# Optimization experiments

Measured on AMD Instinct MI355X. Metric: run time of the kernel, lower is better.

The kernel has to match this reference:

```python
import jax, jax.numpy as jnp
import numpy as np

N = 50000
E = 800000
IN_FEATS = 256
NUM_HEADS = 4
OUT_FEATS = 64
NUM_ETYPES = 8
ALPHA = 100.0
NEG_SLOPE_ATTN = 0.2   # self.leaky_relu
NEG_SLOPE_EW = 0.01    # nn.LeakyReLU() default, applied to edge weights


def leaky_relu(x, slope):
    return jnp.where(x >= 0, x, slope * x)


def setup_inputs() -> dict:
    key = jax.random.key(0)
    ks = jax.random.split(key, 8)
    feat = jax.random.normal(ks[0], (N, IN_FEATS), dtype=jnp.float32)
    src = jax.random.randint(ks[1], (E,), 0, N, dtype=jnp.int32)
    dst = jax.random.randint(ks[2], (E,), 0, N, dtype=jnp.int32)
    # etypes are 1-indexed in the original code (edge_weight[edge_feats - 1])
    edge_feats = jax.random.randint(ks[3], (E,), 1, NUM_ETYPES + 1, dtype=jnp.int32)
    # parameters (xavier-normal-ish init for weights; edge_weight = 1/alpha)
    fc_w = jax.random.normal(ks[4], (NUM_HEADS * OUT_FEATS, IN_FEATS), dtype=jnp.float32) * 0.05
    attn_l = jax.random.normal(ks[5], (1, NUM_HEADS, OUT_FEATS), dtype=jnp.float32) * 0.1
    attn_r = jax.random.normal(ks[6], (1, NUM_HEADS, OUT_FEATS), dtype=jnp.float32) * 0.1
    edge_weight = jnp.full((NUM_ETYPES, NUM_HEADS), 1.0 / ALPHA, dtype=jnp.float32)
    return {"feat": feat, "src": src, "dst": dst, "edge_feats": edge_feats,
            "fc_w": fc_w, "attn_l": attn_l, "attn_r": attn_r, "edge_weight": edge_weight}


def reference(feat, src, dst, edge_feats, fc_w, attn_l, attn_r, edge_weight):
    # feat: [N, F_in] -> ft: [N, H, D]
    ft = (feat @ fc_w.T).reshape(-1, NUM_HEADS, OUT_FEATS)
    el = jnp.einsum('nhd,ohd->nh', ft, attn_l)  # [N, H]
    er = jnp.einsum('nhd,ohd->nh', ft, attn_r)  # [N, H]
    # edge-type weights (1-indexed), scaled & leaky-relu'd
    ew = leaky_relu(edge_weight * ALPHA, NEG_SLOPE_EW)  # [T, H]
    ee = ew[edge_feats - 1]                              # [E, H]
    # per-edge logits: u_add_v, times edge weight, leaky relu
    e = leaky_relu((el[src] + er[dst]) * ee, NEG_SLOPE_ATTN)  # [E, H]
    # edge softmax grouped by destination node
    emax = jax.ops.segment_max(e, dst, num_segments=N)        # [N, H]
    ex = jnp.exp(e - emax[dst])
    denom = jax.ops.segment_sum(ex, dst, num_segments=N)      # [N, H]
    a = ex / denom[dst]                                        # [E, H]
    # weighted scatter-sum: sum over edges of a * ft[src]
    msg = ft[src] * a[:, :, None]                              # [E, H, D]
    rst = jax.ops.segment_sum(msg, dst, num_segments=N)       # [N, H, D]
    return rst
```

## Files before the change

### kernel.cpp

```cpp
#include <hip/hip_runtime.h>
#include <hip/hip_bf16.h>


#define NF 256
#define HD 256
#define NH 4

typedef __attribute__((ext_vector_type(8))) short short8;
typedef __attribute__((ext_vector_type(4))) float f32x4;

static __device__ __forceinline__ unsigned short f2bf(float f) {
  unsigned int u = __float_as_uint(f);
  u += 0x7FFFu + ((u >> 16) & 1u);
  return (unsigned short)(u >> 16);
}
static __device__ __forceinline__ float bf2f(unsigned short s) {
  return __uint_as_float(((unsigned int)s) << 16);
}
static __device__ __forceinline__ unsigned pkbf(float a, float b) {
  __hip_bfloat162 h = __float22bfloat162_rn(make_float2(a, b));
  return *(unsigned*)&h;
}
static __device__ __forceinline__ float wcalc(float sum, float ew) {
  float x = sum * ew;
  x = (x >= 0.f) ? x : 0.2f * x;
  return __expf(x);
}

__global__ __launch_bounds__(256) void hist_cvt_rank_k(
    const int* __restrict__ src, const int* __restrict__ dst,
    const int* __restrict__ efeats, int* __restrict__ cursor,
    int* __restrict__ rkw, const float* __restrict__ w,
    unsigned short* __restrict__ o, int e) {
  int i = blockIdx.x * 256 + threadIdx.x;
  if (i < 16384) {
    float4 v = ((const float4*)w)[i];
    ((uint2*)o)[i] = make_uint2(pkbf(v.x, v.y), pkbf(v.z, v.w));
  }
  if (i < e) {
    int r = atomicAdd(&cursor[dst[i]], 1);
    rkw[i] = src[i] | ((efeats[i] - 1) << 17) | (r << 20);
  }
}

__global__ __launch_bounds__(1024) void scan_k(const int* __restrict__ cursor,
                                               int* __restrict__ offs, int n) {
  __shared__ int wtot[16];
  __shared__ int wexcl[16];
  __shared__ int ctot;
  int tid = threadIdx.x, lane = tid & 63, wid = tid >> 6;
  int carry = 0;
  int nchunk = (n + 8191) >> 13;
  for (int c = 0; c < nchunk; ++c) {
    int base = (c << 13) + tid * 8;
    int v[8];
    if (base + 8 <= n) {
      int4 a = *(const int4*)(cursor + base);
      int4 b = *(const int4*)(cursor + base + 4);
      v[0] = a.x; v[1] = a.y; v[2] = a.z; v[3] = a.w;
      v[4] = b.x; v[5] = b.y; v[6] = b.z; v[7] = b.w;
    } else {
#pragma unroll
      for (int j = 0; j < 8; ++j) v[j] = (base + j < n) ? cursor[base + j] : 0;
    }
    int p[8]; int run = 0;
#pragma unroll
    for (int j = 0; j < 8; ++j) { run += v[j]; p[j] = run; }
    int incl = run;
#pragma unroll
    for (int off = 1; off < 64; off <<= 1) {
      int t = __shfl_up(incl, off);
      if (lane >= off) incl += t;
    }
    if (lane == 63) wtot[wid] = incl;
    __syncthreads();
    if (wid == 0 && lane < 16) {
      int wv = wtot[lane]; int wi = wv;
#pragma unroll
      for (int off = 1; off < 16; off <<= 1) {
        int t = __shfl_up(wi, off);
        if (lane >= off) wi += t;
      }
      wexcl[lane] = wi - wv;
      if (lane == 15) ctot = wi;
    }
    __syncthreads();
    int ebase = carry + wexcl[wid] + (incl - run);
#pragma unroll
    for (int j = 0; j < 8; ++j) {
      int i = base + j;
      if (i < n) offs[i] = ebase + p[j] - v[j];
    }
    carry += ctot;
    __syncthreads();
  }
  if (tid == 0) offs[n] = carry;
}

__global__ __launch_bounds__(256) void gemm_k(
    const float* __restrict__ feat, const unsigned short* __restrict__ fcb,
    const float* __restrict__ attn_l, const float* __restrict__ attn_r,
    unsigned short* __restrict__ ftb, float* __restrict__ el,
    float* __restrict__ er, int n) {
  __shared__ short aF[4 * 2 * 64 * 8];
  __shared__ short bF[16 * 2 * 64 * 8];
  int tid = threadIdx.x;
  int lane = tid & 63, w = tid >> 6;
  int row0 = blockIdx.x * 64;

  f32x4 acc[4][4];
#pragma unroll
  for (int i = 0; i < 4; ++i)
#pragma unroll
    for (int j = 0; j < 4; ++j) acc[i][j] = (f32x4){0.f, 0.f, 0.f, 0.f};

  int ar = tid >> 2, ak = (tid & 3) << 4;
  int arow = row0 + ar; if (arow >= n) arow = n - 1;
  const float* ap = feat + (size_t)arow * NF + ak;
  int am = ar & 15, art = ar >> 4;
  int s0 = ak >> 5, q0 = (ak >> 3) & 3;
  int s1 = (ak + 8) >> 5, q1 = ((ak + 8) >> 3) & 3;
  short* aw0 = &aF[(((art * 2 + s0) * 64) + q0 * 16 + am) * 8];
  short* aw1 = &aF[(((art * 2 + s1) * 64) + q1 * 16 + am) * 8];

  const unsigned short* bp = fcb + (size_t)tid * NF;
  int bn = tid & 15, bcg = tid >> 4;

  for (int k0 = 0; k0 < NF; k0 += 64) {
    float4 f0 = *(const float4*)(ap + k0);
    float4 f1 = *(const float4*)(ap + k0 + 4);
    float4 f2 = *(const float4*)(ap + k0 + 8);
    float4 f3 = *(const float4*)(ap + k0 + 12);
    uint4 oa = make_uint4(pkbf(f0.x, f0.y), pkbf(f0.z, f0.w),
                          pkbf(f1.x, f1.y), pkbf(f1.z, f1.w));
    uint4 ob = make_uint4(pkbf(f2.x, f2.y), pkbf(f2.z, f2.w),
                          pkbf(f3.x, f3.y), pkbf(f3.z, f3.w));
    *(uint4*)aw0 = oa;
    *(uint4*)aw1 = ob;
#pragma unroll
    for (int o8 = 0; o8 < 8; ++o8) {
      short8 bv = *(const short8*)(bp + k0 + o8 * 8);
      int bs = o8 >> 2, bq = o8 & 3;
      *(short8*)&bF[(((bcg * 2 + bs) * 64) + bq * 16 + bn) * 8] = bv;
    }
    __syncthreads();
#pragma unroll
    for (int s = 0; s < 2; ++s) {
      short8 af[4], bfr[4];
#pragma unroll
      for (int rt = 0; rt < 4; ++rt)
        af[rt] = *(const short8*)&aF[(((rt * 2 + s) * 64) + lane) * 8];
#pragma unroll
      for (int ct = 0; ct < 4; ++ct)
        bfr[ct] = *(const short8*)&bF[((((w * 4 + ct) * 2 + s) * 64) + lane) * 8];
#pragma unroll
      for (int rt = 0; rt < 4; ++rt)
#pragma unroll
        for (int ct = 0; ct < 4; ++ct)
          acc[rt][ct] = __builtin_amdgcn_mfma_f32_16x16x32_bf16(
              af[rt], bfr[ct], acc[rt][ct], 0, 0, 0);
    }
    __syncthreads();
  }

  int ln = lane & 15, lq = lane >> 4;
  float al4[4], ar4[4];
#pragma unroll
  for (int ct = 0; ct < 4; ++ct) {
    al4[ct] = attn_l[w * 64 + ct * 16 + ln];
    ar4[ct] = attn_r[w * 64 + ct * 16 + ln];
  }
#pragma unroll
  for (int rt = 0; rt < 4; ++rt) {
#pragma unroll
    for (int r = 0; r < 4; ++r) {
      float pl = 0.f, pr = 0.f;
#pragma unroll
      for (int ct = 0; ct < 4; ++ct) {
        float v = acc[rt][ct][r];
        pl += v * al4[ct]; pr += v * ar4[ct];
      }
#pragma unroll
      for (int off = 1; off <= 8; off <<= 1) {
        pl += __shfl_xor(pl, off);
        pr += __shfl_xor(pr, off);
      }
      int row = row0 + rt * 16 + lq * 4 + r;
      if (row < n) {
        if (ln == 0) { el[row * NH + w] = pl; er[row * NH + w] = pr; }
        unsigned short* fr = ftb + (size_t)row * HD + w * 64 + ln;
#pragma unroll
        for (int ct = 0; ct < 4; ++ct) fr[ct * 16] = f2bf(acc[rt][ct][r]);
      }
    }
  }
}

__global__ __launch_bounds__(256) void pack_k(
    const int* __restrict__ dst, const int* __restrict__ rkw,
    const int* __restrict__ offs, int* __restrict__ pk, int e) {
  int i = blockIdx.x * 256 + threadIdx.x;
  if (i >= e) return;
  unsigned v = (unsigned)rkw[i];
  int p = offs[dst[i]] + (int)(v >> 20);
  pk[p] = (int)(v & 0xFFFFFu);
}

__global__ __launch_bounds__(256) void agg3_k(
    const unsigned short* __restrict__ ftb, const int* __restrict__ pk,
    const float* __restrict__ el, const float* __restrict__ er,
    const float* __restrict__ ewt, const int* __restrict__ offs,
    float* __restrict__ out, int n) {
  __shared__ float ew_s[32];
  if (threadIdx.x < 32) {
    float v = ewt[threadIdx.x] * 100.0f;
    ew_s[threadIdx.x] = (v >= 0.f) ? v : 0.01f * v;
  }
  __syncthreads();
  int node = blockIdx.x * 4 + (threadIdx.x >> 6);
  int lane = threadIdx.x & 63;
  if (node >= n) return;
  int start = offs[node];
  int deg = offs[node + 1] - start;
  float o0 = 0.f, o1 = 0.f, o2 = 0.f, o3 = 0.f;
  if (deg > 0) {
    int hl = lane >> 4;
    float er_h = er[(size_t)node * NH + hl];
    const unsigned short* fb = ftb + (size_t)lane * 4;
    const float* elh = el + hl;
    const int* pg = pk + start;
    float ss = 0.f;
    int i = 0;
    for (; i + 8 <= deg; i += 8) {
      int4 pa = *(const int4*)(pg + i);
      int4 pb = *(const int4*)(pg + i + 4);
      int sA = pa.x & 0x1FFFF, tA = pa.x >> 17;
      int sB = pa.y & 0x1FFFF, tB = pa.y >> 17;
      int sC = pa.z & 0x1FFFF, tC = pa.z >> 17;
      int sD = pa.w & 0x1FFFF, tD = pa.w >> 17;
      int sE = pb.x & 0x1FFFF, tE = pb.x >> 17;
      int sF = pb.y & 0x1FFFF, tF = pb.y >> 17;
      int sG = pb.z & 0x1FFFF, tG = pb.z >> 17;
      int sH = pb.w & 0x1FFFF, tH = pb.w >> 17;
      float eA = elh[sA * NH], eB = elh[sB * NH], eC = elh[sC * NH], eD = elh[sD * NH];
      float eE = elh[sE * NH], eF = elh[sF * NH], eG = elh[sG * NH], eH = elh[sH * NH];
      ushort4 fA = *(const ushort4*)(fb + (size_t)sA * HD);
      ushort4 fB = *(const ushort4*)(fb + (size_t)sB * HD);
      ushort4 fC = *(const ushort4*)(fb + (size_t)sC * HD);
      ushort4 fD = *(const ushort4*)(fb + (size_t)sD * HD);
      ushort4 fE = *(const ushort4*)(fb + (size_t)sE * HD);
      ushort4 fF = *(const ushort4*)(fb + (size_t)sF * HD);
      ushort4 fG = *(const ushort4*)(fb + (size_t)sG * HD);
      ushort4 fH = *(const ushort4*)(fb + (size_t)sH * HD);
      float wA = wcalc(eA + er_h, ew_s[tA * NH + hl]);
      float wB = wcalc(eB + er_h, ew_s[tB * NH + hl]);
      float wC = wcalc(eC + er_h, ew_s[tC * NH + hl]);
      float wD = wcalc(eD + er_h, ew_s[tD * NH + hl]);
      float wE = wcalc(eE + er_h, ew_s[tE * NH + hl]);
      float wF = wcalc(eF + er_h, ew_s[tF * NH + hl]);
      float wG = wcalc(eG + er_h, ew_s[tG * NH + hl]);
      float wH = wcalc(eH + er_h, ew_s[tH * NH + hl]);
      ss += ((wA + wB) + (wC + wD)) + ((wE + wF) + (wG + wH));
      o0 = fmaf(wA, bf2f(fA.x), o0); o1 = fmaf(wA, bf2f(fA.y), o1);
      o2 = fmaf(wA, bf2f(fA.z), o2); o3 = fmaf(wA, bf2f(fA.w), o3);
      o0 = fmaf(wB, bf2f(fB.x), o0); o1 = fmaf(wB, bf2f(fB.y), o1);
      o2 = fmaf(wB, bf2f(fB.z), o2); o3 = fmaf(wB, bf2f(fB.w), o3);
      o0 = fmaf(wC, bf2f(fC.x), o0); o1 = fmaf(wC, bf2f(fC.y), o1);
      o2 = fmaf(wC, bf2f(fC.z), o2); o3 = fmaf(wC, bf2f(fC.w), o3);
      o0 = fmaf(wD, bf2f(fD.x), o0); o1 = fmaf(wD, bf2f(fD.y), o1);
      o2 = fmaf(wD, bf2f(fD.z), o2); o3 = fmaf(wD, bf2f(fD.w), o3);
      o0 = fmaf(wE, bf2f(fE.x), o0); o1 = fmaf(wE, bf2f(fE.y), o1);
      o2 = fmaf(wE, bf2f(fE.z), o2); o3 = fmaf(wE, bf2f(fE.w), o3);
      o0 = fmaf(wF, bf2f(fF.x), o0); o1 = fmaf(wF, bf2f(fF.y), o1);
      o2 = fmaf(wF, bf2f(fF.z), o2); o3 = fmaf(wF, bf2f(fF.w), o3);
      o0 = fmaf(wG, bf2f(fG.x), o0); o1 = fmaf(wG, bf2f(fG.y), o1);
      o2 = fmaf(wG, bf2f(fG.z), o2); o3 = fmaf(wG, bf2f(fG.w), o3);
      o0 = fmaf(wH, bf2f(fH.x), o0); o1 = fmaf(wH, bf2f(fH.y), o1);
      o2 = fmaf(wH, bf2f(fH.z), o2); o3 = fmaf(wH, bf2f(fH.w), o3);
    }
    for (; i < deg; ++i) {
      int pv = pg[i];
      int sA = pv & 0x1FFFF, tA = pv >> 17;
      float eA = elh[sA * NH];
      ushort4 fA = *(const ushort4*)(fb + (size_t)sA * HD);
      float wA = wcalc(eA + er_h, ew_s[tA * NH + hl]);
      ss += wA;
      o0 = fmaf(wA, bf2f(fA.x), o0); o1 = fmaf(wA, bf2f(fA.y), o1);
      o2 = fmaf(wA, bf2f(fA.z), o2); o3 = fmaf(wA, bf2f(fA.w), o3);
    }
    float rs = 1.0f / ss;
    o0 *= rs; o1 *= rs; o2 *= rs; o3 *= rs;
  }
  *(float4*)(out + (size_t)node * HD + lane * 4) = make_float4(o0, o1, o2, o3);
}

extern "C" void kernel_launch(void* const* d_in, const int* in_sizes, int n_in,
                              void* d_out, int out_size, void* d_ws, size_t ws_size,
                              hipStream_t stream) {
  const float* feat   = (const float*)d_in[0];
  const int*   src    = (const int*)d_in[1];
  const int*   dst    = (const int*)d_in[2];
  const int*   efeats = (const int*)d_in[3];
  const float* fc_w   = (const float*)d_in[4];
  const float* attn_l = (const float*)d_in[5];
  const float* attn_r = (const float*)d_in[6];
  const float* ewt    = (const float*)d_in[7];
  float* out = (float*)d_out;

  int N = in_sizes[0] / NF;
  int E = in_sizes[1];

  char* ws = (char*)d_ws;
  size_t off = 0;
  unsigned short* fcb = (unsigned short*)(ws + off); off += (size_t)NF * HD * 2;
  unsigned short* ftb = (unsigned short*)(ws + off); off += (size_t)N * HD * 2;
  float* el  = (float*)(ws + off);  off += (size_t)N * NH * 4;
  float* er  = (float*)(ws + off);  off += (size_t)N * NH * 4;
  int* offs  = (int*)(ws + off);    off += ((size_t)N + 16) * 4;
  int* cursor = (int*)(ws + off);   off += (size_t)N * 4;
  int* rkw   = (int*)(ws + off);    off += (size_t)E * 4;
  int* pk    = (int*)(ws + off);    off += (size_t)E * 4;

  hipMemsetAsync(cursor, 0, (size_t)N * 4, stream);
  hist_cvt_rank_k<<<(E + 255) / 256, 256, 0, stream>>>(src, dst, efeats, cursor,
                                                       rkw, fc_w, fcb, E);
  scan_k<<<1, 1024, 0, stream>>>(cursor, offs, N);
  gemm_k<<<(N + 63) / 64, 256, 0, stream>>>(feat, fcb, attn_l, attn_r, ftb, el, er, N);
  pack_k<<<(E + 255) / 256, 256, 0, stream>>>(dst, rkw, offs, pk, E);
  agg3_k<<<(N + 3) / 4, 256, 0, stream>>>(ftb, pk, el, er, ewt, offs, out, N);
}
```

Measured before the change: 279.9 us.

## Fuse edge histogram into GEMM, pad CSR segments, prefetch in aggregation

The memset plus bf16 weight conversion become a small init kernel. The edge histogram/rank atomics are fused into the GEMM kernel, with each block handling a slice of edges before its matmul tile. This removes a launch and lets the atomic traffic overlap GEMM work. The scan pads each node's segment to a multiple of 8, so the aggregation kernel can drop its scalar tail loop, process masked groups of 8, and prefetch the next index group. In exchange it uses more workspace for padding and extra masking work on partial groups.

```diff
diff --git a/kernel.cpp b/kernel.cpp
--- a/kernel.cpp
+++ b/kernel.cpp
@@ -27,24 +27,133 @@
   return __expf(x);
 }
 
-__global__ __launch_bounds__(256) void hist_cvt_rank_k(
-    const int* __restrict__ src, const int* __restrict__ dst,
-    const int* __restrict__ efeats, int* __restrict__ cursor,
-    int* __restrict__ rkw, const float* __restrict__ w,
-    unsigned short* __restrict__ o, int e) {
+__global__ __launch_bounds__(256) void init_k(
+    const float* __restrict__ w, unsigned short* __restrict__ o,
+    int* __restrict__ cursor, int n) {
   int i = blockIdx.x * 256 + threadIdx.x;
   if (i < 16384) {
     float4 v = ((const float4*)w)[i];
     ((uint2*)o)[i] = make_uint2(pkbf(v.x, v.y), pkbf(v.z, v.w));
   }
-  if (i < e) {
-    int r = atomicAdd(&cursor[dst[i]], 1);
-    rkw[i] = src[i] | ((efeats[i] - 1) << 17) | (r << 20);
+  int nq = n >> 2;
+  if (i < nq) ((int4*)cursor)[i] = make_int4(0, 0, 0, 0);
+  int t = nq * 4 + i;
+  if (i < (n & 3)) cursor[t] = 0;
+}
+
+__global__ __launch_bounds__(256) void gemm_hist_k(
+    const float* __restrict__ feat, const unsigned short* __restrict__ fcb,
+    const float* __restrict__ attn_l, const float* __restrict__ attn_r,
+    unsigned short* __restrict__ ftb, float* __restrict__ el,
+    float* __restrict__ er, int n,
+    const int* __restrict__ src, const int* __restrict__ dst,
+    const int* __restrict__ efeats, int* __restrict__ cursor,
+    int* __restrict__ rkw, int e, int epb) {
+  {
+    int e0 = blockIdx.x * epb;
+    int e1 = e0 + epb; if (e1 > e) e1 = e;
+    for (int i = e0 + threadIdx.x; i < e1; i += 256) {
+      int r = atomicAdd(&cursor[dst[i]], 1);
+      rkw[i] = src[i] | ((efeats[i] - 1) << 17) | (r << 20);
+    }
+  }
+
+  __shared__ short aF[4 * 2 * 64 * 8];
+  __shared__ short bF[16 * 2 * 64 * 8];
+  int tid = threadIdx.x;
+  int lane = tid & 63, w = tid >> 6;
+  int row0 = blockIdx.x * 64;
+
+  f32x4 acc[4][4];
+#pragma unroll
+  for (int i = 0; i < 4; ++i)
+#pragma unroll
+    for (int j = 0; j < 4; ++j) acc[i][j] = (f32x4){0.f, 0.f, 0.f, 0.f};
+
+  int ar = tid >> 2, ak = (tid & 3) << 4;
+  int arow = row0 + ar; if (arow >= n) arow = n - 1;
+  const float* ap = feat + (size_t)arow * NF + ak;
+  int am = ar & 15, art = ar >> 4;
+  int s0 = ak >> 5, q0 = (ak >> 3) & 3;
+  int s1 = (ak + 8) >> 5, q1 = ((ak + 8) >> 3) & 3;
+  short* aw0 = &aF[(((art * 2 + s0) * 64) + q0 * 16 + am) * 8];
+  short* aw1 = &aF[(((art * 2 + s1) * 64) + q1 * 16 + am) * 8];
+
+  const unsigned short* bp = fcb + (size_t)tid * NF;
+  int bn = tid & 15, bcg = tid >> 4;
+
+  for (int k0 = 0; k0 < NF; k0 += 64) {
+    float4 f0 = *(const float4*)(ap + k0);
+    float4 f1 = *(const float4*)(ap + k0 + 4);
+    float4 f2 = *(const float4*)(ap + k0 + 8);
+    float4 f3 = *(const float4*)(ap + k0 + 12);
+    uint4 oa = make_uint4(pkbf(f0.x, f0.y), pkbf(f0.z, f0.w),
+                          pkbf(f1.x, f1.y), pkbf(f1.z, f1.w));
+    uint4 ob = make_uint4(pkbf(f2.x, f2.y), pkbf(f2.z, f2.w),
+                          pkbf(f3.x, f3.y), pkbf(f3.z, f3.w));
+    *(uint4*)aw0 = oa;
+    *(uint4*)aw1 = ob;
+#pragma unroll
+    for (int o8 = 0; o8 < 8; ++o8) {
+      short8 bv = *(const short8*)(bp + k0 + o8 * 8);
+      int bs = o8 >> 2, bq = o8 & 3;
+      *(short8*)&bF[(((bcg * 2 + bs) * 64) + bq * 16 + bn) * 8] = bv;
+    }
+    __syncthreads();
+#pragma unroll
+    for (int s = 0; s < 2; ++s) {
+      short8 af[4], bfr[4];
+#pragma unroll
+      for (int rt = 0; rt < 4; ++rt)
+        af[rt] = *(const short8*)&aF[(((rt * 2 + s) * 64) + lane) * 8];
+#pragma unroll
+      for (int ct = 0; ct < 4; ++ct)
+        bfr[ct] = *(const short8*)&bF[((((w * 4 + ct) * 2 + s) * 64) + lane) * 8];
+#pragma unroll
+      for (int rt = 0; rt < 4; ++rt)
+#pragma unroll
+        for (int ct = 0; ct < 4; ++ct)
+          acc[rt][ct] = __builtin_amdgcn_mfma_f32_16x16x32_bf16(
+              af[rt], bfr[ct], acc[rt][ct], 0, 0, 0);
+    }
+    __syncthreads();
+  }
+
+  int ln = lane & 15, lq = lane >> 4;
+  float al4[4], ar4[4];
+#pragma unroll
+  for (int ct = 0; ct < 4; ++ct) {
+    al4[ct] = attn_l[w * 64 + ct * 16 + ln];
+    ar4[ct] = attn_r[w * 64 + ct * 16 + ln];
+  }
+#pragma unroll
+  for (int rt = 0; rt < 4; ++rt) {
+#pragma unroll
+    for (int r = 0; r < 4; ++r) {
+      float pl = 0.f, pr = 0.f;
+#pragma unroll
+      for (int ct = 0; ct < 4; ++ct) {
+        float v = acc[rt][ct][r];
+        pl += v * al4[ct]; pr += v * ar4[ct];
+      }
+#pragma unroll
+      for (int off = 1; off <= 8; off <<= 1) {
+        pl += __shfl_xor(pl, off);
+        pr += __shfl_xor(pr, off);
+      }
+      int row = row0 + rt * 16 + lq * 4 + r;
+      if (row < n) {
+        if (ln == 0) { el[row * NH + w] = pl; er[row * NH + w] = pr; }
+        unsigned short* fr = ftb + (size_t)row * HD + w * 64 + ln;
+#pragma unroll
+        for (int ct = 0; ct < 4; ++ct) fr[ct * 16] = f2bf(acc[rt][ct][r]);
+      }
+    }
   }
 }
 
 __global__ __launch_bounds__(1024) void scan_k(const int* __restrict__ cursor,
-                                               int* __restrict__ offs, int n) {
+                                               int* __restrict__ poffs, int n) {
   __shared__ int wtot[16];
   __shared__ int wexcl[16];
   __shared__ int ctot;
@@ -63,6 +172,8 @@
 #pragma unroll
       for (int j = 0; j < 8; ++j) v[j] = (base + j < n) ? cursor[base + j] : 0;
     }
+#pragma unroll
+    for (int j = 0; j < 8; ++j) v[j] = (v[j] + 7) & ~7;
     int p[8]; int run = 0;
 #pragma unroll
     for (int j = 0; j < 8; ++j) { run += v[j]; p[j] = run; }
@@ -89,128 +200,29 @@
 #pragma unroll
     for (int j = 0; j < 8; ++j) {
       int i = base + j;
-      if (i < n) offs[i] = ebase + p[j] - v[j];
+      if (i < n) poffs[i] = ebase + p[j] - v[j];
     }
     carry += ctot;
     __syncthreads();
   }
-  if (tid == 0) offs[n] = carry;
-}
-
-__global__ __launch_bounds__(256) void gemm_k(
-    const float* __restrict__ feat, const unsigned short* __restrict__ fcb,
-    const float* __restrict__ attn_l, const float* __restrict__ attn_r,
-    unsigned short* __restrict__ ftb, float* __restrict__ el,
-    float* __restrict__ er, int n) {
-  __shared__ short aF[4 * 2 * 64 * 8];
-  __shared__ short bF[16 * 2 * 64 * 8];
-  int tid = threadIdx.x;
-  int lane = tid & 63, w = tid >> 6;
-  int row0 = blockIdx.x * 64;
-
-  f32x4 acc[4][4];
-#pragma unroll
-  for (int i = 0; i < 4; ++i)
-#pragma unroll
-    for (int j = 0; j < 4; ++j) acc[i][j] = (f32x4){0.f, 0.f, 0.f, 0.f};
-
-  int ar = tid >> 2, ak = (tid & 3) << 4;
-  int arow = row0 + ar; if (arow >= n) arow = n - 1;
-  const float* ap = feat + (size_t)arow * NF + ak;
-  int am = ar & 15, art = ar >> 4;
-  int s0 = ak >> 5, q0 = (ak >> 3) & 3;
-  int s1 = (ak + 8) >> 5, q1 = ((ak + 8) >> 3) & 3;
-  short* aw0 = &aF[(((art * 2 + s0) * 64) + q0 * 16 + am) * 8];
-  short* aw1 = &aF[(((art * 2 + s1) * 64) + q1 * 16 + am) * 8];
-
-  const unsigned short* bp = fcb + (size_t)tid * NF;
-  int bn = tid & 15, bcg = tid >> 4;
-
-  for (int k0 = 0; k0 < NF; k0 += 64) {
-    float4 f0 = *(const float4*)(ap + k0);
-    float4 f1 = *(const float4*)(ap + k0 + 4);
-    float4 f2 = *(const float4*)(ap + k0 + 8);
-    float4 f3 = *(const float4*)(ap + k0 + 12);
-    uint4 oa = make_uint4(pkbf(f0.x, f0.y), pkbf(f0.z, f0.w),
-                          pkbf(f1.x, f1.y), pkbf(f1.z, f1.w));
-    uint4 ob = make_uint4(pkbf(f2.x, f2.y), pkbf(f2.z, f2.w),
-                          pkbf(f3.x, f3.y), pkbf(f3.z, f3.w));
-    *(uint4*)aw0 = oa;
-    *(uint4*)aw1 = ob;
-#pragma unroll
-    for (int o8 = 0; o8 < 8; ++o8) {
-      short8 bv = *(const short8*)(bp + k0 + o8 * 8);
-      int bs = o8 >> 2, bq = o8 & 3;
-      *(short8*)&bF[(((bcg * 2 + bs) * 64) + bq * 16 + bn) * 8] = bv;
-    }
-    __syncthreads();
-#pragma unroll
-    for (int s = 0; s < 2; ++s) {
-      short8 af[4], bfr[4];
-#pragma unroll
-      for (int rt = 0; rt < 4; ++rt)
-        af[rt] = *(const short8*)&aF[(((rt * 2 + s) * 64) + lane) * 8];
-#pragma unroll
-      for (int ct = 0; ct < 4; ++ct)
-        bfr[ct] = *(const short8*)&bF[((((w * 4 + ct) * 2 + s) * 64) + lane) * 8];
-#pragma unroll
-      for (int rt = 0; rt < 4; ++rt)
-#pragma unroll
-        for (int ct = 0; ct < 4; ++ct)
-          acc[rt][ct] = __builtin_amdgcn_mfma_f32_16x16x32_bf16(
-              af[rt], bfr[ct], acc[rt][ct], 0, 0, 0);
-    }
-    __syncthreads();
-  }
-
-  int ln = lane & 15, lq = lane >> 4;
-  float al4[4], ar4[4];
-#pragma unroll
-  for (int ct = 0; ct < 4; ++ct) {
-    al4[ct] = attn_l[w * 64 + ct * 16 + ln];
-    ar4[ct] = attn_r[w * 64 + ct * 16 + ln];
-  }
-#pragma unroll
-  for (int rt = 0; rt < 4; ++rt) {
-#pragma unroll
-    for (int r = 0; r < 4; ++r) {
-      float pl = 0.f, pr = 0.f;
-#pragma unroll
-      for (int ct = 0; ct < 4; ++ct) {
-        float v = acc[rt][ct][r];
-        pl += v * al4[ct]; pr += v * ar4[ct];
-      }
-#pragma unroll
-      for (int off = 1; off <= 8; off <<= 1) {
-        pl += __shfl_xor(pl, off);
-        pr += __shfl_xor(pr, off);
-      }
-      int row = row0 + rt * 16 + lq * 4 + r;
-      if (row < n) {
-        if (ln == 0) { el[row * NH + w] = pl; er[row * NH + w] = pr; }
-        unsigned short* fr = ftb + (size_t)row * HD + w * 64 + ln;
-#pragma unroll
-        for (int ct = 0; ct < 4; ++ct) fr[ct * 16] = f2bf(acc[rt][ct][r]);
-      }
-    }
-  }
+  if (tid == 0) poffs[n] = carry;
 }
 
 __global__ __launch_bounds__(256) void pack_k(
     const int* __restrict__ dst, const int* __restrict__ rkw,
-    const int* __restrict__ offs, int* __restrict__ pk, int e) {
+    const int* __restrict__ poffs, int* __restrict__ pk, int e) {
   int i = blockIdx.x * 256 + threadIdx.x;
   if (i >= e) return;
   unsigned v = (unsigned)rkw[i];
-  int p = offs[dst[i]] + (int)(v >> 20);
+  int p = poffs[dst[i]] + (int)(v >> 20);
   pk[p] = (int)(v & 0xFFFFFu);
 }
 
-__global__ __launch_bounds__(256) void agg3_k(
+__global__ __launch_bounds__(256) void agg4_k(
     const unsigned short* __restrict__ ftb, const int* __restrict__ pk,
     const float* __restrict__ el, const float* __restrict__ er,
-    const float* __restrict__ ewt, const int* __restrict__ offs,
-    float* __restrict__ out, int n) {
+    const float* __restrict__ ewt, const int* __restrict__ poffs,
+    const int* __restrict__ cnt, float* __restrict__ out, int n) {
   __shared__ float ew_s[32];
   if (threadIdx.x < 32) {
     float v = ewt[threadIdx.x] * 100.0f;
@@ -220,8 +232,8 @@
   int node = blockIdx.x * 4 + (threadIdx.x >> 6);
   int lane = threadIdx.x & 63;
   if (node >= n) return;
-  int start = offs[node];
-  int deg = offs[node + 1] - start;
+  int start = poffs[node];
+  int deg = cnt[node];
   float o0 = 0.f, o1 = 0.f, o2 = 0.f, o3 = 0.f;
   if (deg > 0) {
     int hl = lane >> 4;
@@ -230,10 +242,22 @@
     const float* elh = el + hl;
     const int* pg = pk + start;
     float ss = 0.f;
-    int i = 0;
-    for (; i + 8 <= deg; i += 8) {
-      int4 pa = *(const int4*)(pg + i);
-      int4 pb = *(const int4*)(pg + i + 4);
+    int ng = (deg + 7) >> 3;
+    int4 pa = *(const int4*)(pg);
+    int4 pb = *(const int4*)(pg + 4);
+    for (int g = 0; g < ng; ++g) {
+      int4 na = *(const int4*)(pg + (g + 1) * 8);
+      int4 nb = *(const int4*)(pg + (g + 1) * 8 + 4);
+      int rem = deg - (g << 3);
+      if (rem < 8) {
+        pa.y = (rem > 1) ? pa.y : 0;
+        pa.z = (rem > 2) ? pa.z : 0;
+        pa.w = (rem > 3) ? pa.w : 0;
+        pb.x = (rem > 4) ? pb.x : 0;
+        pb.y = (rem > 5) ? pb.y : 0;
+        pb.z = (rem > 6) ? pb.z : 0;
+        pb.w = (rem > 7) ? pb.w : 0;
+      }
       int sA = pa.x & 0x1FFFF, tA = pa.x >> 17;
       int sB = pa.y & 0x1FFFF, tB = pa.y >> 17;
       int sC = pa.z & 0x1FFFF, tC = pa.z >> 17;
@@ -260,6 +284,15 @@
       float wF = wcalc(eF + er_h, ew_s[tF * NH + hl]);
       float wG = wcalc(eG + er_h, ew_s[tG * NH + hl]);
       float wH = wcalc(eH + er_h, ew_s[tH * NH + hl]);
+      if (rem < 8) {
+        wB = (rem > 1) ? wB : 0.f;
+        wC = (rem > 2) ? wC : 0.f;
+        wD = (rem > 3) ? wD : 0.f;
+        wE = (rem > 4) ? wE : 0.f;
+        wF = (rem > 5) ? wF : 0.f;
+        wG = (rem > 6) ? wG : 0.f;
+        wH = (rem > 7) ? wH : 0.f;
+      }
       ss += ((wA + wB) + (wC + wD)) + ((wE + wF) + (wG + wH));
       o0 = fmaf(wA, bf2f(fA.x), o0); o1 = fmaf(wA, bf2f(fA.y), o1);
       o2 = fmaf(wA, bf2f(fA.z), o2); o3 = fmaf(wA, bf2f(fA.w), o3);
@@ -277,16 +310,7 @@
       o2 = fmaf(wG, bf2f(fG.z), o2); o3 = fmaf(wG, bf2f(fG.w), o3);
       o0 = fmaf(wH, bf2f(fH.x), o0); o1 = fmaf(wH, bf2f(fH.y), o1);
       o2 = fmaf(wH, bf2f(fH.z), o2); o3 = fmaf(wH, bf2f(fH.w), o3);
-    }
-    for (; i < deg; ++i) {
-      int pv = pg[i];
-      int sA = pv & 0x1FFFF, tA = pv >> 17;
-      float eA = elh[sA * NH];
-      ushort4 fA = *(const ushort4*)(fb + (size_t)sA * HD);
-      float wA = wcalc(eA + er_h, ew_s[tA * NH + hl]);
-      ss += wA;
-      o0 = fmaf(wA, bf2f(fA.x), o0); o1 = fmaf(wA, bf2f(fA.y), o1);
-      o2 = fmaf(wA, bf2f(fA.z), o2); o3 = fmaf(wA, bf2f(fA.w), o3);
+      pa = na; pb = nb;
     }
     float rs = 1.0f / ss;
     o0 *= rs; o1 *= rs; o2 *= rs; o3 *= rs;
@@ -316,16 +340,18 @@
   unsigned short* ftb = (unsigned short*)(ws + off); off += (size_t)N * HD * 2;
   float* el  = (float*)(ws + off);  off += (size_t)N * NH * 4;
   float* er  = (float*)(ws + off);  off += (size_t)N * NH * 4;
-  int* offs  = (int*)(ws + off);    off += ((size_t)N + 16) * 4;
+  int* poffs = (int*)(ws + off);    off += ((size_t)N + 16) * 4;
   int* cursor = (int*)(ws + off);   off += (size_t)N * 4;
   int* rkw   = (int*)(ws + off);    off += (size_t)E * 4;
-  int* pk    = (int*)(ws + off);    off += (size_t)E * 4;
-
-  hipMemsetAsync(cursor, 0, (size_t)N * 4, stream);
-  hist_cvt_rank_k<<<(E + 255) / 256, 256, 0, stream>>>(src, dst, efeats, cursor,
-                                                       rkw, fc_w, fcb, E);
-  scan_k<<<1, 1024, 0, stream>>>(cursor, offs, N);
-  gemm_k<<<(N + 63) / 64, 256, 0, stream>>>(feat, fcb, attn_l, attn_r, ftb, el, er, N);
-  pack_k<<<(E + 255) / 256, 256, 0, stream>>>(dst, rkw, offs, pk, E);
-  agg3_k<<<(N + 3) / 4, 256, 0, stream>>>(ftb, pk, el, er, ewt, offs, out, N);
-}
+  int* pk    = (int*)(ws + off);    off += ((size_t)E + 7 * (size_t)N + 64) * 4;
+
+  int gblocks = (N + 63) / 64;
+  int epb = (E + gblocks - 1) / gblocks;
+
+  init_k<<<64, 256, 0, stream>>>(fc_w, fcb, cursor, N);
+  gemm_hist_k<<<gblocks, 256, 0, stream>>>(feat, fcb, attn_l, attn_r, ftb, el, er, N,
+                                           src, dst, efeats, cursor, rkw, E, epb);
+  scan_k<<<1, 1024, 0, stream>>>(cursor, poffs, N);
+  pack_k<<<(E + 255) / 256, 256, 0, stream>>>(dst, rkw, poffs, pk, E);
+  agg4_k<<<(N + 3) / 4, 256, 0, stream>>>(ftb, pk, el, er, ewt, poffs, cursor, out, N);
+}
```

Result: no change. 280.0 us (+0.1%).
